# Kernel tuning notes

Measured on AMD Instinct MI355X. Metric: run time of the kernel, lower is better.

Reference implementation:

```python
import jax, jax.numpy as jnp
import numpy as np


def setup_inputs() -> dict:
    key = jax.random.key(0)
    k1, k2, k3 = jax.random.split(key, 3)
    B, C, H, W = 64, 256, 32, 32   # batch, hidden_dim, latent grid
    D, K = 128, 1024               # latent_dim, num_embeddings
    z = jax.random.normal(k1, (B, C, H, W), dtype=jnp.float32)
    proj_w = jax.random.normal(k2, (D, C), dtype=jnp.float32) * 0.02  # 1x1 conv kernel [out,in]
    proj_b = jnp.zeros((D,), jnp.float32)
    # codebook init uniform(-1/K, 1/K) as in torch module
    embed = (jax.random.uniform(k3, (K, D), dtype=jnp.float32) * 2.0 - 1.0) / K
    return {"z": z, "proj_w": proj_w, "proj_b": proj_b, "embed": embed}


def reference(z, proj_w, proj_b, embed):
    # 1x1 conv projection: [B,C,H,W] -> [B,H,W,D]  (fuses conv + permute)
    zp = jnp.einsum('bchw,dc->bhwd', z, proj_w) + proj_b
    B, H, W, D = zp.shape
    zf = zp.reshape(-1, D)                                   # [N, D], N = B*H*W
    # squared Euclidean distance to codebook: ||z||^2 - 2 z.e + ||e||^2  -> [N, K]
    dist = (jnp.sum(zf * zf, axis=1, keepdims=True)
            - 2.0 * (zf @ embed.T)
            + jnp.sum(embed * embed, axis=1))
    min_indices = jnp.argmin(dist, axis=1)                   # [N]
    z_q = embed[min_indices].reshape(B, H, W, D)             # codebook gather
    # straight-through estimator
    rep_z_q = zp + jax.lax.stop_gradient(z_q - zp)
    rep_z_q = rep_z_q.transpose(0, 3, 1, 2)                  # back to NCHW
    return rep_z_q, min_indices
```

## Files before the change

kernel.cpp:

```cpp
#include <hip/hip_runtime.h>

#define B_   64
#define C_   256
#define D_   128
#define HW_  1024
#define K_   1024
#define N_   65536
#define MARGIN_PREF 1.2e-3f

typedef __attribute__((ext_vector_type(8))) short short8;
typedef __attribute__((ext_vector_type(4))) float f32x4;

__device__ __forceinline__ unsigned short f2bf(float f) {
    unsigned u = __float_as_uint(f);
    return (unsigned short)((u + 0x7FFFu + ((u >> 16) & 1u)) >> 16);
}
__device__ __forceinline__ unsigned long long packdk(float d, int k) {
    unsigned u = __float_as_uint(d);
    u = (u & 0x80000000u) ? ~u : (u | 0x80000000u);
    return ((unsigned long long)u << 10) | (unsigned)k;
}
__device__ __forceinline__ unsigned long long min64(unsigned long long a, unsigned long long b) {
    return a < b ? a : b;
}

template <typename F>
__device__ __forceinline__ float np_sum128(F ld) {
#pragma clang fp contract(off)
    float r0 = ld(0), r1 = ld(1), r2 = ld(2), r3 = ld(3);
    float r4 = ld(4), r5 = ld(5), r6 = ld(6), r7 = ld(7);
#pragma unroll
    for (int i = 8; i < 128; i += 8) {
        r0 = r0 + ld(i + 0); r1 = r1 + ld(i + 1);
        r2 = r2 + ld(i + 2); r3 = r3 + ld(i + 3);
        r4 = r4 + ld(i + 4); r5 = r5 + ld(i + 5);
        r6 = r6 + ld(i + 6); r7 = r7 + ld(i + 7);
    }
    return ((r0 + r1) + (r2 + r3)) + ((r4 + r5) + (r6 + r7));
}

__global__ __launch_bounds__(256) void k0_norms(const float* __restrict__ embed,
                                                float* __restrict__ enorm,
                                                unsigned short* __restrict__ ebf) {
#pragma clang fp contract(off)
    int k = blockIdx.x * 256 + threadIdx.x;
    if (k >= K_) return;
    const float* e = embed + (size_t)k * D_;
    enorm[k] = np_sum128([&](int i) { float v = e[i]; return v * v; });
    const int sw = (k & 7) << 4;
    char* rowp = (char*)ebf + ((size_t)k << 8);
#pragma unroll
    for (int j = 0; j < 16; ++j) {
        short8 v;
#pragma unroll
        for (int q = 0; q < 8; ++q) v[q] = (short)f2bf(e[j * 8 + q]);
        *(short8*)(rowp + ((j * 16) ^ sw)) = v;
    }
}

__global__ __launch_bounds__(256) void k1_proj(const float* __restrict__ z,
                                               const float* __restrict__ w,
                                               const float* __restrict__ bias,
                                               float* __restrict__ zp,
                                               unsigned short* __restrict__ zbf) {
#pragma clang fp contract(off)
    __shared__ float zs[64][64];
    __shared__ float wsh[64][128];
    const int b   = blockIdx.x >> 4;
    const int hw0 = (blockIdx.x & 15) << 6;
    const int t   = threadIdx.x;
    const int hwg = (t & 7) * 8;
    const int dg  = (t >> 3) * 4;

    float acc[8][4];
#pragma unroll
    for (int i = 0; i < 8; ++i)
#pragma unroll
        for (int j = 0; j < 4; ++j) acc[i][j] = 0.f;

    for (int ct = 0; ct < C_; ct += 64) {
        __syncthreads();
#pragma unroll
        for (int i = 0; i < 16; ++i) {
            int idx = i * 256 + t;
            int cc = idx >> 6, hwl = idx & 63;
            zs[cc][hwl] = z[(((size_t)b * C_ + ct + cc) << 10) + hw0 + hwl];
        }
#pragma unroll
        for (int i = 0; i < 32; ++i) {
            int idx = i * 256 + t;
            int cc = idx >> 7, d = idx & 127;
            wsh[cc][d] = w[(size_t)d * C_ + ct + cc];
        }
        __syncthreads();
#pragma unroll 2
        for (int cc = 0; cc < 64; ++cc) {
            float4 za = *(const float4*)&zs[cc][hwg];
            float4 zb = *(const float4*)&zs[cc][hwg + 4];
            float4 wv = *(const float4*)&wsh[cc][dg];
            float zv[8]  = {za.x, za.y, za.z, za.w, zb.x, zb.y, zb.z, zb.w};
            float wva[4] = {wv.x, wv.y, wv.z, wv.w};
#pragma unroll
            for (int i = 0; i < 8; ++i)
#pragma unroll
                for (int j = 0; j < 4; ++j) {
                    float p = zv[i] * wva[j];
                    acc[i][j] = acc[i][j] + p;
                }
        }
    }
#pragma unroll
    for (int i = 0; i < 8; ++i)
#pragma unroll
        for (int j = 0; j < 4; ++j) {
            float v = acc[i][j] + bias[dg + j];
            size_t off = (((size_t)b * HW_ + hw0 + hwg + i) << 7) + dg + j;
            zp[off]  = v;
            zbf[off] = f2bf(v);
        }
}

__global__ __launch_bounds__(256) void k0z_znorm(const float* __restrict__ zp,
                                                 float* __restrict__ znorm) {
#pragma clang fp contract(off)
    __shared__ float zl[64][129];
    const int t = threadIdx.x, n0 = blockIdx.x * 64;
#pragma unroll
    for (int i = 0; i < 32; ++i) {
        int idx = i * 256 + t;
        zl[idx >> 7][idx & 127] = zp[(size_t)n0 * 128 + idx];
    }
    __syncthreads();
    if (t < 64)
        znorm[n0 + t] = np_sum128([&](int i) { float v = zl[t][i]; return v * v; });
}

__global__ __launch_bounds__(256) void k2_argmin(const unsigned short* __restrict__ zbf,
                                                 const unsigned short* __restrict__ ebf,
                                                 const float* __restrict__ zp,
                                                 const float* __restrict__ embed,
                                                 const float* __restrict__ enorm,
                                                 const float* __restrict__ znorm,
                                                 int* __restrict__ bestk_ws,
                                                 float* __restrict__ out_idx) {
    __shared__ unsigned char etile[2][32 * 256];
    __shared__ float els[1024];
    const int t   = threadIdx.x;
    const int l   = t & 63;
    const int wid = t >> 6;
    const int r0  = (blockIdx.x * 4 + wid) * 16;
    const int lr  = l & 15;
    const int lh  = l >> 4;

    short8 zfrag[4];
#pragma unroll
    for (int dt = 0; dt < 4; ++dt) {
        zfrag[dt] = *(const short8*)(zbf + (((size_t)(r0 + lr)) << 7) + dt * 32 + lh * 8);
        asm volatile("" : "+v"(zfrag[dt]));
    }

    const int swz = (lr & 7) << 4;
    int roff[4];
#pragma unroll
    for (int dt = 0; dt < 4; ++dt)
        roff[dt] = lr * 256 + ((dt * 64 + lh * 16) ^ swz);

    const char* ebf_b   = (const char*)ebf;
    const int   stg_off = wid * 1024;

    auto STAGE = [&](int st, int b) {
#pragma unroll
        for (int j = 0; j < 2; ++j) {
            int off = j * 4096 + stg_off;
            __builtin_amdgcn_global_load_lds(
                (const __attribute__((address_space(1))) void*)(ebf_b + ((size_t)st << 13) + off + (l << 4)),
                (__attribute__((address_space(3))) void*)(&etile[b][off]),
                16, 0, 0);
        }
    };

#pragma unroll
    for (int i = 0; i < 4; ++i) els[i * 256 + t] = enorm[i * 256 + t];

    float bmin = 1e30f;
    STAGE(0, 0);
#pragma unroll 1
    for (int st = 0; st < 32; ++st) {
        __syncthreads();
        if (st < 31) STAGE(st + 1, (st + 1) & 1);
        const unsigned char* buf = etile[st & 1];
#pragma unroll
        for (int ks = 0; ks < 2; ++ks) {
            short8 af[4];
#pragma unroll
            for (int dt = 0; dt < 4; ++dt)
                af[dt] = *(const short8*)(buf + ks * 4096 + roff[dt]);
            f32x4 en4 = *(const f32x4*)(els + st * 32 + ks * 16 + lh * 4);
            f32x4 acc = {0.f, 0.f, 0.f, 0.f};
#pragma unroll
            for (int dt = 0; dt < 4; ++dt)
                acc = __builtin_amdgcn_mfma_f32_16x16x32_bf16(af[dt], zfrag[dt], acc, 0, 0, 0);
#pragma unroll
            for (int reg = 0; reg < 4; ++reg)
                bmin = fminf(bmin, fmaf(-2.f, acc[reg], en4[reg]));
        }
    }
    {
        bmin = fminf(bmin, __shfl_xor(bmin, 16, 64));
        bmin = fminf(bmin, __shfl_xor(bmin, 32, 64));
    }
    const float thr = bmin + MARGIN_PREF;

    unsigned long long ca = 0, cb = 0;
    int cnt = 0;
    __syncthreads();
    STAGE(0, 0);
#pragma unroll 1
    for (int st = 0; st < 32; ++st) {
        __syncthreads();
        if (st < 31) STAGE(st + 1, (st + 1) & 1);
        const unsigned char* buf = etile[st & 1];
#pragma unroll
        for (int ks = 0; ks < 2; ++ks) {
            short8 af[4];
#pragma unroll
            for (int dt = 0; dt < 4; ++dt)
                af[dt] = *(const short8*)(buf + ks * 4096 + roff[dt]);
            f32x4 en4 = *(const f32x4*)(els + st * 32 + ks * 16 + lh * 4);
            f32x4 acc = {0.f, 0.f, 0.f, 0.f};
#pragma unroll
            for (int dt = 0; dt < 4; ++dt)
                acc = __builtin_amdgcn_mfma_f32_16x16x32_bf16(af[dt], zfrag[dt], acc, 0, 0, 0);
#pragma unroll
            for (int reg = 0; reg < 4; ++reg) {
                float dist = fmaf(-2.f, acc[reg], en4[reg]);
                if (dist < thr) {
                    int kk = st * 32 + ks * 16 + lh * 4 + reg;
                    if (cnt < 6)       ca |= (unsigned long long)kk << (10 * cnt);
                    else if (cnt < 12) cb |= (unsigned long long)kk << (10 * (cnt - 6));
                    ++cnt;
                }
            }
        }
    }

    const int myrow = r0 + lr;
    const float* zrow = zp + ((size_t)myrow << 7);
    const float  zn   = znorm[myrow];
    unsigned long long best = ~0ull;

    auto refine = [&](int kk) {
#pragma clang fp contract(off)
        const float* e = embed + ((size_t)kk << 7);
        float s = 0.f;
#pragma unroll 1
        for (int d = 0; d < 128; ++d) s = fmaf(zrow[d], e[d], s);
        float T  = 2.0f * s;
        float A  = zn - T;
        float Bv = A + enorm[kk];
        best = min64(best, packdk(Bv, kk));
    };

    if (cnt <= 12) {
#pragma unroll
        for (int i = 0; i < 6; ++i)
            if (i < cnt) refine((int)((ca >> (10 * i)) & 1023ull));
#pragma unroll
        for (int i = 6; i < 12; ++i)
            if (i < cnt) refine((int)((cb >> (10 * (i - 6))) & 1023ull));
    } else {
#pragma unroll 1
        for (int kt = 0; kt < 64; ++kt)
#pragma unroll
            for (int reg = 0; reg < 4; ++reg) refine(kt * 16 + lh * 4 + reg);
    }
    {
        unsigned long long o;
        o = __shfl_xor(best, 16, 64); best = min64(best, o);
        o = __shfl_xor(best, 32, 64); best = min64(best, o);
    }
    if (l < 16) {
        int kk = (int)(best & 1023ull);
        bestk_ws[r0 + l] = kk;
        out_idx[r0 + l]  = (float)kk;
    }
}

__global__ __launch_bounds__(256) void k3_gather(const float* __restrict__ embed,
                                                 const int* __restrict__ bestk,
                                                 float* __restrict__ out0) {
    __shared__ float tile[64][129];
    const int b   = blockIdx.x >> 4;
    const int hw0 = (blockIdx.x & 15) << 6;
    const int t   = threadIdx.x;
    const int n0  = b * HW_ + hw0;
#pragma unroll
    for (int i = 0; i < 32; ++i) {
        int idx = i * 256 + t;
        int hwl = idx >> 7, d = idx & 127;
        int k = bestk[n0 + hwl];
        tile[hwl][d] = embed[(size_t)k * 128 + d];
    }
    __syncthreads();
#pragma unroll
    for (int i = 0; i < 32; ++i) {
        int idx = i * 256 + t;
        int d = idx >> 6, hwl = idx & 63;
        out0[(((size_t)b * D_ + d) << 10) + hw0 + hwl] = tile[hwl][d];
    }
}

extern "C" void kernel_launch(void* const* d_in, const int* in_sizes, int n_in,
                              void* d_out, int out_size, void* d_ws, size_t ws_size,
                              hipStream_t stream) {
    const float* z     = (const float*)d_in[0];
    const float* pw    = (const float*)d_in[1];
    const float* pb    = (const float*)d_in[2];
    const float* embed = (const float*)d_in[3];

    float* out0 = (float*)d_out;
    float* out1 = (float*)d_out + (size_t)B_ * D_ * HW_;

    char* ws = (char*)d_ws;
    float*          zp    = (float*)ws;
    unsigned short* zbf   = (unsigned short*)(ws + (32u << 20));
    unsigned short* ebf   = (unsigned short*)(ws + (48u << 20));
    float*          enorm = (float*)(ws + (48u << 20) + (256u << 10));
    float*          znorm = (float*)(ws + (49u << 20));
    int*            bestk = (int*)  (ws + (50u << 20));

    hipLaunchKernelGGL(k0_norms,  dim3(4),    dim3(256), 0, stream, embed, enorm, ebf);
    hipLaunchKernelGGL(k1_proj,   dim3(1024), dim3(256), 0, stream, z, pw, pb, zp, zbf);
    hipLaunchKernelGGL(k0z_znorm, dim3(1024), dim3(256), 0, stream, zp, znorm);
    hipLaunchKernelGGL(k2_argmin, dim3(1024), dim3(256), 0, stream,
                       zbf, ebf, zp, embed, enorm, znorm, bestk, out1);
    hipLaunchKernelGGL(k3_gather, dim3(1024), dim3(256), 0, stream, embed, bestk, out0);
}
```

Baseline: 372.7 us.

## Give each wave a private codebook staging buffer and drop block barriers

Each wave now streams the whole bf16 codebook into its own double-buffered LDS region in 16-row tiles. It waits with explicit vmcnt counters instead of __syncthreads, which removes the block-wide barrier from each stage of both argmin passes. The cost is four times the global/L2 traffic for codebook staging and four times the LDS footprint (32KB), which may lower occupancy. It also relies on the vmcnt accounting being correct for LDS-direct loads.

```diff
diff --git a/kernel.cpp b/kernel.cpp
--- a/kernel.cpp
+++ b/kernel.cpp
@@ -143,7 +143,7 @@
                                                  const float* __restrict__ znorm,
                                                  int* __restrict__ bestk_ws,
                                                  float* __restrict__ out_idx) {
-    __shared__ unsigned char etile[2][32 * 256];
+    __shared__ unsigned char wbuf[4][2][4096];
     __shared__ float els[1024];
     const int t   = threadIdx.x;
     const int l   = t & 63;
@@ -165,46 +165,50 @@
     for (int dt = 0; dt < 4; ++dt)
         roff[dt] = lr * 256 + ((dt * 64 + lh * 16) ^ swz);
 
-    const char* ebf_b   = (const char*)ebf;
-    const int   stg_off = wid * 1024;
-
-    auto STAGE = [&](int st, int b) {
-#pragma unroll
-        for (int j = 0; j < 2; ++j) {
-            int off = j * 4096 + stg_off;
+#pragma unroll
+    for (int i = 0; i < 4; ++i) els[i * 256 + t] = enorm[i * 256 + t];
+    __syncthreads();
+
+    const char* ebf_b = (const char*)ebf;
+    auto STAGE = [&](int tile, int b) {
+#pragma unroll
+        for (int j = 0; j < 4; ++j) {
             __builtin_amdgcn_global_load_lds(
-                (const __attribute__((address_space(1))) void*)(ebf_b + ((size_t)st << 13) + off + (l << 4)),
-                (__attribute__((address_space(3))) void*)(&etile[b][off]),
+                (const __attribute__((address_space(1))) void*)(ebf_b + ((size_t)tile << 12) + j * 1024 + (l << 4)),
+                (__attribute__((address_space(3))) void*)(&wbuf[wid][b][j * 1024 + (l << 4)]),
                 16, 0, 0);
         }
     };
 
-#pragma unroll
-    for (int i = 0; i < 4; ++i) els[i * 256 + t] = enorm[i * 256 + t];
-
     float bmin = 1e30f;
-    STAGE(0, 0);
+    auto computeA = [&](int tile, const unsigned char* buf) {
+        short8 af[4];
+#pragma unroll
+        for (int dt = 0; dt < 4; ++dt)
+            af[dt] = *(const short8*)(buf + roff[dt]);
+        f32x4 en4 = *(const f32x4*)(els + tile * 16 + lh * 4);
+        f32x4 acc = {0.f, 0.f, 0.f, 0.f};
+#pragma unroll
+        for (int dt = 0; dt < 4; ++dt)
+            acc = __builtin_amdgcn_mfma_f32_16x16x32_bf16(af[dt], zfrag[dt], acc, 0, 0, 0);
+#pragma unroll
+        for (int reg = 0; reg < 4; ++reg)
+            bmin = fminf(bmin, fmaf(-2.f, acc[reg], en4[reg]));
+    };
+
+    STAGE(0, 0); STAGE(1, 1);
 #pragma unroll 1
-    for (int st = 0; st < 32; ++st) {
-        __syncthreads();
-        if (st < 31) STAGE(st + 1, (st + 1) & 1);
-        const unsigned char* buf = etile[st & 1];
-#pragma unroll
-        for (int ks = 0; ks < 2; ++ks) {
-            short8 af[4];
-#pragma unroll
-            for (int dt = 0; dt < 4; ++dt)
-                af[dt] = *(const short8*)(buf + ks * 4096 + roff[dt]);
-            f32x4 en4 = *(const f32x4*)(els + st * 32 + ks * 16 + lh * 4);
-            f32x4 acc = {0.f, 0.f, 0.f, 0.f};
-#pragma unroll
-            for (int dt = 0; dt < 4; ++dt)
-                acc = __builtin_amdgcn_mfma_f32_16x16x32_bf16(af[dt], zfrag[dt], acc, 0, 0, 0);
-#pragma unroll
-            for (int reg = 0; reg < 4; ++reg)
-                bmin = fminf(bmin, fmaf(-2.f, acc[reg], en4[reg]));
-        }
-    }
+    for (int tt = 0; tt < 63; ++tt) {
+        asm volatile("s_waitcnt vmcnt(4)" ::: "memory");
+        __builtin_amdgcn_sched_barrier(0);
+        computeA(tt, wbuf[wid][tt & 1]);
+        __builtin_amdgcn_sched_barrier(0);
+        if (tt < 62) STAGE(tt + 2, tt & 1);
+    }
+    asm volatile("s_waitcnt vmcnt(0)" ::: "memory");
+    __builtin_amdgcn_sched_barrier(0);
+    computeA(63, wbuf[wid][1]);
+
     {
         bmin = fminf(bmin, __shfl_xor(bmin, 16, 64));
         bmin = fminf(bmin, __shfl_xor(bmin, 32, 64));
@@ -213,36 +217,40 @@
 
     unsigned long long ca = 0, cb = 0;
     int cnt = 0;
-    __syncthreads();
-    STAGE(0, 0);
+    auto computeB = [&](int tile, const unsigned char* buf) {
+        short8 af[4];
+#pragma unroll
+        for (int dt = 0; dt < 4; ++dt)
+            af[dt] = *(const short8*)(buf + roff[dt]);
+        f32x4 en4 = *(const f32x4*)(els + tile * 16 + lh * 4);
+        f32x4 acc = {0.f, 0.f, 0.f, 0.f};
+#pragma unroll
+        for (int dt = 0; dt < 4; ++dt)
+            acc = __builtin_amdgcn_mfma_f32_16x16x32_bf16(af[dt], zfrag[dt], acc, 0, 0, 0);
+#pragma unroll
+        for (int reg = 0; reg < 4; ++reg) {
+            float dist = fmaf(-2.f, acc[reg], en4[reg]);
+            if (dist < thr) {
+                int kk = tile * 16 + lh * 4 + reg;
+                if (cnt < 6)       ca |= (unsigned long long)kk << (10 * cnt);
+                else if (cnt < 12) cb |= (unsigned long long)kk << (10 * (cnt - 6));
+                ++cnt;
+            }
+        }
+    };
+
+    STAGE(0, 0); STAGE(1, 1);
 #pragma unroll 1
-    for (int st = 0; st < 32; ++st) {
-        __syncthreads();
-        if (st < 31) STAGE(st + 1, (st + 1) & 1);
-        const unsigned char* buf = etile[st & 1];
-#pragma unroll
-        for (int ks = 0; ks < 2; ++ks) {
-            short8 af[4];
-#pragma unroll
-            for (int dt = 0; dt < 4; ++dt)
-                af[dt] = *(const short8*)(buf + ks * 4096 + roff[dt]);
-            f32x4 en4 = *(const f32x4*)(els + st * 32 + ks * 16 + lh * 4);
-            f32x4 acc = {0.f, 0.f, 0.f, 0.f};
-#pragma unroll
-            for (int dt = 0; dt < 4; ++dt)
-                acc = __builtin_amdgcn_mfma_f32_16x16x32_bf16(af[dt], zfrag[dt], acc, 0, 0, 0);
-#pragma unroll
-            for (int reg = 0; reg < 4; ++reg) {
-                float dist = fmaf(-2.f, acc[reg], en4[reg]);
-                if (dist < thr) {
-                    int kk = st * 32 + ks * 16 + lh * 4 + reg;
-                    if (cnt < 6)       ca |= (unsigned long long)kk << (10 * cnt);
-                    else if (cnt < 12) cb |= (unsigned long long)kk << (10 * (cnt - 6));
-                    ++cnt;
-                }
-            }
-        }
-    }
+    for (int tt = 0; tt < 63; ++tt) {
+        asm volatile("s_waitcnt vmcnt(4)" ::: "memory");
+        __builtin_amdgcn_sched_barrier(0);
+        computeB(tt, wbuf[wid][tt & 1]);
+        __builtin_amdgcn_sched_barrier(0);
+        if (tt < 62) STAGE(tt + 2, tt & 1);
+    }
+    asm volatile("s_waitcnt vmcnt(0)" ::: "memory");
+    __builtin_amdgcn_sched_barrier(0);
+    computeB(63, wbuf[wid][1]);
 
     const int myrow = r0 + lr;
     const float* zrow = zp + ((size_t)myrow << 7);
```

After: 407.6 us. +9.4%, slower.
